# Performance work log

Measured on AMD Instinct MI355X. Metric: run time of the kernel, lower is better.

## Reference

```python
import jax, jax.numpy as jnp
import numpy as np

DIM = 512
HEADS = 8
DIM_HEAD = 64
INNER = HEADS * DIM_HEAD
SCALE = DIM_HEAD ** -0.5


def setup_inputs() -> dict:
    key = jax.random.key(0)
    ks = jax.random.split(key, 7)
    B, N = 8, 1024
    x = jax.random.normal(ks[0], (B, N, DIM), dtype=jnp.float32)
    rel_pos_bias = jax.random.normal(ks[1], (HEADS, N, N), dtype=jnp.float32) * 0.02
    w_qkv = jax.random.normal(ks[2], (DIM, 3 * INNER), dtype=jnp.float32) * (DIM ** -0.5)
    w_out = jax.random.normal(ks[3], (INNER, DIM), dtype=jnp.float32) * (INNER ** -0.5)
    b_out = jnp.zeros((DIM,), dtype=jnp.float32)
    ln_gamma = jnp.ones((DIM,), dtype=jnp.float32)
    ln_beta = jnp.zeros((DIM,), dtype=jnp.float32)
    return {"x": x, "rel_pos_bias": rel_pos_bias, "w_qkv": w_qkv,
            "w_out": w_out, "b_out": b_out, "ln_gamma": ln_gamma, "ln_beta": ln_beta}


def _layernorm(x, gamma, beta, eps=1e-5):
    mu = jnp.mean(x, axis=-1, keepdims=True)
    var = jnp.var(x, axis=-1, keepdims=True)
    return (x - mu) * jax.lax.rsqrt(var + eps) * gamma + beta


def reference(x, rel_pos_bias, w_qkv, w_out, b_out, ln_gamma, ln_beta):
    B, N, _ = x.shape
    xn = _layernorm(x, ln_gamma, ln_beta)
    qkv = xn @ w_qkv  # [B,N,3*INNER]
    q, k, v = jnp.split(qkv, 3, axis=-1)
    # b n (h d) -> b h n d
    reshape = lambda t: t.reshape(B, N, HEADS, DIM_HEAD).transpose(0, 2, 1, 3)
    q, k, v = reshape(q) * SCALE, reshape(k), reshape(v)
    sim = jnp.einsum('bhid,bhjd->bhij', q, k)
    sim = sim + rel_pos_bias  # broadcast [h,N,N] over batch
    attn = jax.nn.softmax(sim, axis=-1)
    out = jnp.einsum('bhij,bhjd->bhid', attn, v)
    out = out.transpose(0, 2, 1, 3).reshape(B, N, INNER)
    return out @ w_out + b_out
```

## Files before the change

### kernel.cpp

```cpp
#include <hip/hip_runtime.h>
#include <hip/hip_bf16.h>

#define DIM 512
#define HEADS 8
#define DHEAD 64
#define INNER 512
#define NSEQ 1024
#define BATCH 8
#define MROWS (BATCH*NSEQ)
#define QK_SCALE 0.125f

typedef __attribute__((ext_vector_type(4))) float f32x4;
typedef __attribute__((ext_vector_type(8))) short short8;
typedef unsigned short ushort_t;

__device__ inline ushort_t f2bf(float f) {
    __hip_bfloat16 h = __float2bfloat16(f);
    return *reinterpret_cast<ushort_t*>(&h);
}

__global__ __launch_bounds__(256) void ln_kernel(const float* __restrict__ x,
        const float* __restrict__ gamma, const float* __restrict__ beta,
        ushort_t* __restrict__ xn) {
    int row = blockIdx.x * 4 + (threadIdx.x >> 6);
    int lane = threadIdx.x & 63;
    const float4* xr = (const float4*)(x + (size_t)row * DIM);
    float4 a0 = xr[lane];
    float4 a1 = xr[lane + 64];
    float s  = a0.x + a0.y + a0.z + a0.w + a1.x + a1.y + a1.z + a1.w;
    float ss = a0.x*a0.x + a0.y*a0.y + a0.z*a0.z + a0.w*a0.w
             + a1.x*a1.x + a1.y*a1.y + a1.z*a1.z + a1.w*a1.w;
    for (int off = 1; off < 64; off <<= 1) {
        s  += __shfl_xor(s, off);
        ss += __shfl_xor(ss, off);
    }
    float mean = s * (1.0f / DIM);
    float var  = ss * (1.0f / DIM) - mean * mean;
    float inv  = rsqrtf(var + 1e-5f);
    const float4* g4 = (const float4*)gamma;
    const float4* b4 = (const float4*)beta;
    float4 g0 = g4[lane], g1 = g4[lane + 64];
    float4 be0 = b4[lane], be1 = b4[lane + 64];
    ushort4 o0, o1;
    o0.x = f2bf((a0.x - mean) * inv * g0.x + be0.x);
    o0.y = f2bf((a0.y - mean) * inv * g0.y + be0.y);
    o0.z = f2bf((a0.z - mean) * inv * g0.z + be0.z);
    o0.w = f2bf((a0.w - mean) * inv * g0.w + be0.w);
    o1.x = f2bf((a1.x - mean) * inv * g1.x + be1.x);
    o1.y = f2bf((a1.y - mean) * inv * g1.y + be1.y);
    o1.z = f2bf((a1.z - mean) * inv * g1.z + be1.z);
    o1.w = f2bf((a1.w - mean) * inv * g1.w + be1.w);
    ushort4* outr = (ushort4*)(xn + (size_t)row * DIM);
    outr[lane] = o0;
    outr[lane + 64] = o1;
}

__global__ __launch_bounds__(256) void transpose_cast(const float* __restrict__ w,
        ushort_t* __restrict__ wt, int ncols) {
    int idx = blockIdx.x * 256 + threadIdx.x;
    int n = idx >> 9, k = idx & 511;
    wt[idx] = f2bf(w[(size_t)k * ncols + n]);
}

template<int EPI>
__global__ __launch_bounds__(256) void gemm_kernel(
        const ushort_t* __restrict__ A, const ushort_t* __restrict__ Bt,
        ushort_t* __restrict__ qb, ushort_t* __restrict__ kb, ushort_t* __restrict__ vb,
        float* __restrict__ outp, const float* __restrict__ bvec) {
    __shared__ ushort_t Als[128][40];
    __shared__ ushort_t Bls[128][40];
    int t = threadIdx.x;
    int bm = blockIdx.y, bn = blockIdx.x;
    int lane = t & 63, w = t >> 6, wm = w >> 1, wn = w & 1;
    int l15 = lane & 15, l4 = lane >> 4;
    f32x4 acc[4][4] = {};

    for (int kt = 0; kt < DIM / 32; ++kt) {
        __syncthreads();
        {
            int row = t >> 2, c8 = (t & 3) * 8;
            uint4 va0 = *(const uint4*)(A  + (size_t)(bm*128 + row)      * DIM + kt*32 + c8);
            uint4 va1 = *(const uint4*)(A  + (size_t)(bm*128 + row + 64) * DIM + kt*32 + c8);
            uint4 vb0 = *(const uint4*)(Bt + (size_t)(bn*128 + row)      * DIM + kt*32 + c8);
            uint4 vb1 = *(const uint4*)(Bt + (size_t)(bn*128 + row + 64) * DIM + kt*32 + c8);
            *(uint4*)&Als[row][c8]      = va0;
            *(uint4*)&Als[row + 64][c8] = va1;
            *(uint4*)&Bls[row][c8]      = vb0;
            *(uint4*)&Bls[row + 64][c8] = vb1;
        }
        __syncthreads();
        short8 af[4], bfr[4];
        for (int mi = 0; mi < 4; mi++) af[mi]  = *(const short8*)&Als[wm*64 + mi*16 + l15][l4*8];
        for (int ni = 0; ni < 4; ni++) bfr[ni] = *(const short8*)&Bls[wn*64 + ni*16 + l15][l4*8];
        for (int mi = 0; mi < 4; mi++)
            for (int ni = 0; ni < 4; ni++)
                acc[mi][ni] = __builtin_amdgcn_mfma_f32_16x16x32_bf16(af[mi], bfr[ni], acc[mi][ni], 0, 0, 0);
    }

    int rbase = bm*128 + wm*64 + l4*4;
    int cbase = bn*128 + wn*64 + l15;
    for (int mi = 0; mi < 4; mi++)
        for (int ni = 0; ni < 4; ni++) {
            int c = cbase + ni*16;
            for (int j = 0; j < 4; j++) {
                int r = rbase + mi*16 + j;
                float val = acc[mi][ni][j];
                if (EPI == 0) {
                    int part = c >> 9, cw = c & 511;
                    int h = cw >> 6, d = cw & 63;
                    int b = r >> 10, i = r & 1023;
                    size_t off = (((size_t)(b*HEADS + h)) * NSEQ + i) * DHEAD + d;
                    if (part == 0)      qb[off] = f2bf(val * QK_SCALE);
                    else if (part == 1) kb[off] = f2bf(val);
                    else                vb[off] = f2bf(val);
                } else {
                    outp[(size_t)r * DIM + c] = val + bvec[c];
                }
            }
        }
}

__global__ __launch_bounds__(256) void attn_kernel(
        const ushort_t* __restrict__ q, const ushort_t* __restrict__ k,
        const ushort_t* __restrict__ v, const float* __restrict__ bias,
        ushort_t* __restrict__ attno) {
    __shared__ ushort_t Kls[64][72];
    __shared__ ushort_t Vtls[64][72];
    __shared__ ushort_t Pls[4][16][72];
    int t = threadIdx.x, lane = t & 63, w = t >> 6;
    int l15 = lane & 15, l4 = lane >> 4;
    int b = blockIdx.z, h = blockIdx.y, q0 = blockIdx.x * 64;
    const ushort_t* qp = q + (((size_t)(b*HEADS + h)) * NSEQ + q0 + w*16) * DHEAD;
    const ushort_t* kp = k + ((size_t)(b*HEADS + h)) * NSEQ * DHEAD;
    const ushort_t* vp = v + ((size_t)(b*HEADS + h)) * NSEQ * DHEAD;
    const float* bp = bias + (size_t)h * NSEQ * NSEQ;

    short8 aq[2];
    aq[0] = *(const short8*)(qp + l15*DHEAD + l4*8);
    aq[1] = *(const short8*)(qp + l15*DHEAD + l4*8 + 32);

    f32x4 o[4] = {};
    float mrun[4], lrun[4];
    for (int j = 0; j < 4; j++) { mrun[j] = -INFINITY; lrun[j] = 0.f; }
    int rbase = q0 + w*16 + l4*4;

    for (int kt = 0; kt < NSEQ / 64; ++kt) {
        __syncthreads();
        {
            int row = t >> 3, c8 = (t & 7) * 8;
            for (int r2 = 0; r2 < 2; ++r2) {
                int rr = row + r2*32;
                uint4 kv4 = *(const uint4*)(kp + (size_t)(kt*64 + rr) * DHEAD + c8);
                *(uint4*)&Kls[rr][c8] = kv4;
                uint4 vv4 = *(const uint4*)(vp + (size_t)(kt*64 + rr) * DHEAD + c8);
                ushort_t* vs = (ushort_t*)&vv4;
                for (int jj = 0; jj < 8; jj++) Vtls[c8 + jj][rr] = vs[jj];
            }
        }
        __syncthreads();

        f32x4 s[4] = {};
        for (int ni = 0; ni < 4; ni++)
            for (int ks = 0; ks < 2; ks++) {
                short8 bk = *(const short8*)&Kls[ni*16 + l15][l4*8 + 32*ks];
                s[ni] = __builtin_amdgcn_mfma_f32_16x16x32_bf16(aq[ks], bk, s[ni], 0, 0, 0);
            }

        float pv[4][4];
        const float* bpp = bp + (size_t)rbase * NSEQ + kt*64 + l15;
        for (int j = 0; j < 4; j++) {
            float mj = -INFINITY;
            for (int ni = 0; ni < 4; ni++) {
                float val = s[ni][j] + bpp[(size_t)j * NSEQ + ni*16];
                pv[ni][j] = val;
                mj = fmaxf(mj, val);
            }
            for (int off = 1; off < 16; off <<= 1) mj = fmaxf(mj, __shfl_xor(mj, off));
            float mnew = fmaxf(mrun[j], mj);
            float scl = __expf(mrun[j] - mnew);
            float rs = 0.f;
            for (int ni = 0; ni < 4; ni++) {
                float p = __expf(pv[ni][j] - mnew);
                pv[ni][j] = p;
                rs += p;
            }
            for (int off = 1; off < 16; off <<= 1) rs += __shfl_xor(rs, off);
            lrun[j] = lrun[j] * scl + rs;
            mrun[j] = mnew;
            for (int di = 0; di < 4; di++) o[di][j] *= scl;
        }

        for (int ni = 0; ni < 4; ni++)
            for (int j = 0; j < 4; j++)
                Pls[w][l4*4 + j][ni*16 + l15] = f2bf(pv[ni][j]);

        for (int ks = 0; ks < 2; ks++) {
            short8 pa = *(const short8*)&Pls[w][l15][l4*8 + 32*ks];
            for (int di = 0; di < 4; di++) {
                short8 bv = *(const short8*)&Vtls[di*16 + l15][l4*8 + 32*ks];
                o[di] = __builtin_amdgcn_mfma_f32_16x16x32_bf16(pa, bv, o[di], 0, 0, 0);
            }
        }
    }

    for (int di = 0; di < 4; di++)
        for (int j = 0; j < 4; j++) {
            int row = rbase + j;
            float val = o[di][j] / lrun[j];
            attno[((size_t)(b*NSEQ + row)) * INNER + h*DHEAD + di*16 + l15] = f2bf(val);
        }
}

extern "C" void kernel_launch(void* const* d_in, const int* in_sizes, int n_in,
                              void* d_out, int out_size, void* d_ws, size_t ws_size,
                              hipStream_t stream) {
    (void)in_sizes; (void)n_in; (void)out_size; (void)ws_size;
    const float* x      = (const float*)d_in[0];
    const float* bias   = (const float*)d_in[1];
    const float* w_qkv  = (const float*)d_in[2];
    const float* w_out  = (const float*)d_in[3];
    const float* b_out  = (const float*)d_in[4];
    const float* gamma  = (const float*)d_in[5];
    const float* beta   = (const float*)d_in[6];
    float* out = (float*)d_out;

    ushort_t* xn    = (ushort_t*)d_ws;
    ushort_t* wqkvT = xn + (size_t)MROWS * DIM;
    ushort_t* woutT = wqkvT + (size_t)1536 * 512;
    ushort_t* qb    = woutT + (size_t)512 * 512;
    ushort_t* kb    = qb + (size_t)MROWS * INNER;
    ushort_t* vb    = kb + (size_t)MROWS * INNER;
    ushort_t* attn  = vb + (size_t)MROWS * INNER;

    hipLaunchKernelGGL(ln_kernel, dim3(MROWS / 4), dim3(256), 0, stream, x, gamma, beta, xn);
    hipLaunchKernelGGL(transpose_cast, dim3(1536 * 512 / 256), dim3(256), 0, stream, w_qkv, wqkvT, 3 * INNER);
    hipLaunchKernelGGL(transpose_cast, dim3(512 * 512 / 256), dim3(256), 0, stream, w_out, woutT, DIM);
    hipLaunchKernelGGL((gemm_kernel<0>), dim3(1536 / 128, MROWS / 128), dim3(256), 0, stream,
                       xn, wqkvT, qb, kb, vb, nullptr, nullptr);
    hipLaunchKernelGGL(attn_kernel, dim3(NSEQ / 64, HEADS, BATCH), dim3(256), 0, stream,
                       qb, kb, vb, bias, attn);
    hipLaunchKernelGGL((gemm_kernel<1>), dim3(DIM / 128, MROWS / 128), dim3(256), 0, stream,
                       attn, woutT, nullptr, nullptr, nullptr, out, b_out);
}
```

Baseline: 225.2 us.

## Transpose attention MFMAs, pre-transpose V, and pre-convert bias to bf16

Swaps the MFMA operand roles in the attention kernel so each lane owns a whole query row. Row max and sum then need only two cross-lane shuffles, and bias loads become vectorized ushort4 reads along the key dimension. A separate kernel pre-transposes V into [bh, d, seq] layout, which replaces the scalar LDS transpose scatter with vector copies. Another kernel converts the rel_pos_bias to bf16 once per call, halving bias read traffic in attention. The cost is two extra launches and a full fp32 pass over the bias, plus bf16 rounding of the bias.

```diff
diff --git a/kernel.cpp b/kernel.cpp
--- a/kernel.cpp
+++ b/kernel.cpp
@@ -17,6 +17,9 @@
 __device__ inline ushort_t f2bf(float f) {
     __hip_bfloat16 h = __float2bfloat16(f);
     return *reinterpret_cast<ushort_t*>(&h);
+}
+__device__ inline float bf2f(ushort_t u) {
+    union { unsigned int i; float f; } c; c.i = ((unsigned int)u) << 16; return c.f;
 }
 
 __global__ __launch_bounds__(256) void ln_kernel(const float* __restrict__ x,
@@ -62,6 +65,34 @@
     wt[idx] = f2bf(w[(size_t)k * ncols + n]);
 }
 
+__global__ __launch_bounds__(256) void bias_cvt(const float* __restrict__ in,
+        ushort_t* __restrict__ out) {
+    int i = blockIdx.x * 256 + threadIdx.x;
+    float4 v = ((const float4*)in)[i];
+    ushort4 o;
+    o.x = f2bf(v.x); o.y = f2bf(v.y); o.z = f2bf(v.z); o.w = f2bf(v.w);
+    ((ushort4*)out)[i] = o;
+}
+
+__global__ __launch_bounds__(256) void v_transpose(const ushort_t* __restrict__ vb,
+        ushort_t* __restrict__ vt) {
+    __shared__ ushort_t T[64][72];
+    int bh = blockIdx.y;
+    int s0 = blockIdx.x * 64;
+    int t = threadIdx.x;
+    int row = t >> 2, c = (t & 3) * 16;
+    const ushort_t* src = vb + ((size_t)bh * NSEQ + s0 + row) * DHEAD + c;
+    *(uint4*)&T[row][c]     = *(const uint4*)(src);
+    *(uint4*)&T[row][c + 8] = *(const uint4*)(src + 8);
+    __syncthreads();
+    int d = t >> 2;
+    int sq = (t & 3) * 16;
+    ushort_t tmp[16];
+    for (int j = 0; j < 16; j++) tmp[j] = T[sq + j][d];
+    *(uint4*)(vt + ((size_t)bh * DHEAD + d) * NSEQ + s0 + sq)     = *(uint4*)&tmp[0];
+    *(uint4*)(vt + ((size_t)bh * DHEAD + d) * NSEQ + s0 + sq + 8) = *(uint4*)&tmp[8];
+}
+
 template<int EPI>
 __global__ __launch_bounds__(256) void gemm_kernel(
         const ushort_t* __restrict__ A, const ushort_t* __restrict__ Bt,
@@ -122,7 +153,7 @@
 
 __global__ __launch_bounds__(256) void attn_kernel(
         const ushort_t* __restrict__ q, const ushort_t* __restrict__ k,
-        const ushort_t* __restrict__ v, const float* __restrict__ bias,
+        const ushort_t* __restrict__ vt, const ushort_t* __restrict__ biasb,
         ushort_t* __restrict__ attno) {
     __shared__ ushort_t Kls[64][72];
     __shared__ ushort_t Vtls[64][72];
@@ -130,85 +161,95 @@
     int t = threadIdx.x, lane = t & 63, w = t >> 6;
     int l15 = lane & 15, l4 = lane >> 4;
     int b = blockIdx.z, h = blockIdx.y, q0 = blockIdx.x * 64;
-    const ushort_t* qp = q + (((size_t)(b*HEADS + h)) * NSEQ + q0 + w*16) * DHEAD;
-    const ushort_t* kp = k + ((size_t)(b*HEADS + h)) * NSEQ * DHEAD;
-    const ushort_t* vp = v + ((size_t)(b*HEADS + h)) * NSEQ * DHEAD;
-    const float* bp = bias + (size_t)h * NSEQ * NSEQ;
-
-    short8 aq[2];
-    aq[0] = *(const short8*)(qp + l15*DHEAD + l4*8);
-    aq[1] = *(const short8*)(qp + l15*DHEAD + l4*8 + 32);
+    size_t bh = (size_t)(b * HEADS + h);
+    const ushort_t* qp = q  + (bh * NSEQ + q0 + w*16) * DHEAD;
+    const ushort_t* kp = k  + bh * NSEQ * DHEAD;
+    const ushort_t* vp = vt + bh * DHEAD * NSEQ;
+    int qrow = q0 + w*16 + l15;
+    const ushort_t* bp = biasb + ((size_t)h * NSEQ + qrow) * NSEQ;
+
+    short8 bq[2];
+    bq[0] = *(const short8*)(qp + l15*DHEAD + l4*8);
+    bq[1] = *(const short8*)(qp + l15*DHEAD + l4*8 + 32);
 
     f32x4 o[4] = {};
-    float mrun[4], lrun[4];
-    for (int j = 0; j < 4; j++) { mrun[j] = -INFINITY; lrun[j] = 0.f; }
-    int rbase = q0 + w*16 + l4*4;
+    float mrun = -INFINITY, lrun = 0.f;
+
+    int srow = t >> 2, sc = (t & 3) * 16;
 
     for (int kt = 0; kt < NSEQ / 64; ++kt) {
         __syncthreads();
         {
-            int row = t >> 3, c8 = (t & 7) * 8;
-            for (int r2 = 0; r2 < 2; ++r2) {
-                int rr = row + r2*32;
-                uint4 kv4 = *(const uint4*)(kp + (size_t)(kt*64 + rr) * DHEAD + c8);
-                *(uint4*)&Kls[rr][c8] = kv4;
-                uint4 vv4 = *(const uint4*)(vp + (size_t)(kt*64 + rr) * DHEAD + c8);
-                ushort_t* vs = (ushort_t*)&vv4;
-                for (int jj = 0; jj < 8; jj++) Vtls[c8 + jj][rr] = vs[jj];
+            const ushort_t* ks = kp + (size_t)(kt*64 + srow) * DHEAD + sc;
+            const ushort_t* vs = vp + (size_t)srow * NSEQ + kt*64 + sc;
+            *(uint4*)&Kls[srow][sc]      = *(const uint4*)(ks);
+            *(uint4*)&Kls[srow][sc + 8]  = *(const uint4*)(ks + 8);
+            *(uint4*)&Vtls[srow][sc]     = *(const uint4*)(vs);
+            *(uint4*)&Vtls[srow][sc + 8] = *(const uint4*)(vs + 8);
+        }
+        __syncthreads();
+
+        f32x4 s[4];
+        for (int ni = 0; ni < 4; ni++) {
+            f32x4 z = {};
+            short8 ak0 = *(const short8*)&Kls[ni*16 + l15][l4*8];
+            short8 ak1 = *(const short8*)&Kls[ni*16 + l15][l4*8 + 32];
+            z = __builtin_amdgcn_mfma_f32_16x16x32_bf16(ak0, bq[0], z, 0, 0, 0);
+            z = __builtin_amdgcn_mfma_f32_16x16x32_bf16(ak1, bq[1], z, 0, 0, 0);
+            s[ni] = z;
+        }
+
+        float p[16];
+        float mj = -INFINITY;
+        for (int ni = 0; ni < 4; ni++) {
+            ushort4 b4 = *(const ushort4*)(bp + kt*64 + ni*16 + l4*4);
+            float v0 = s[ni][0] + bf2f(b4.x);
+            float v1 = s[ni][1] + bf2f(b4.y);
+            float v2 = s[ni][2] + bf2f(b4.z);
+            float v3 = s[ni][3] + bf2f(b4.w);
+            p[ni*4+0] = v0; p[ni*4+1] = v1; p[ni*4+2] = v2; p[ni*4+3] = v3;
+            mj = fmaxf(mj, fmaxf(fmaxf(v0, v1), fmaxf(v2, v3)));
+        }
+        mj = fmaxf(mj, __shfl_xor(mj, 16));
+        mj = fmaxf(mj, __shfl_xor(mj, 32));
+        float mnew = fmaxf(mrun, mj);
+        float scl = __expf(mrun - mnew);
+        float rs = 0.f;
+        for (int i = 0; i < 16; i++) {
+            p[i] = __expf(p[i] - mnew);
+            rs += p[i];
+        }
+        rs += __shfl_xor(rs, 16);
+        rs += __shfl_xor(rs, 32);
+        lrun = lrun * scl + rs;
+        mrun = mnew;
+        for (int di = 0; di < 4; di++) o[di] *= scl;
+
+        for (int ni = 0; ni < 4; ni++) {
+            ushort4 pk;
+            pk.x = f2bf(p[ni*4+0]); pk.y = f2bf(p[ni*4+1]);
+            pk.z = f2bf(p[ni*4+2]); pk.w = f2bf(p[ni*4+3]);
+            *(ushort4*)&Pls[w][l15][ni*16 + l4*4] = pk;
+        }
+
+        for (int ks2 = 0; ks2 < 2; ks2++) {
+            short8 pb = *(const short8*)&Pls[w][l15][ks2*32 + l4*8];
+            for (int di = 0; di < 4; di++) {
+                short8 av = *(const short8*)&Vtls[di*16 + l15][ks2*32 + l4*8];
+                o[di] = __builtin_amdgcn_mfma_f32_16x16x32_bf16(av, pb, o[di], 0, 0, 0);
             }
         }
-        __syncthreads();
-
-        f32x4 s[4] = {};
-        for (int ni = 0; ni < 4; ni++)
-            for (int ks = 0; ks < 2; ks++) {
-                short8 bk = *(const short8*)&Kls[ni*16 + l15][l4*8 + 32*ks];
-                s[ni] = __builtin_amdgcn_mfma_f32_16x16x32_bf16(aq[ks], bk, s[ni], 0, 0, 0);
-            }
-
-        float pv[4][4];
-        const float* bpp = bp + (size_t)rbase * NSEQ + kt*64 + l15;
-        for (int j = 0; j < 4; j++) {
-            float mj = -INFINITY;
-            for (int ni = 0; ni < 4; ni++) {
-                float val = s[ni][j] + bpp[(size_t)j * NSEQ + ni*16];
-                pv[ni][j] = val;
-                mj = fmaxf(mj, val);
-            }
-            for (int off = 1; off < 16; off <<= 1) mj = fmaxf(mj, __shfl_xor(mj, off));
-            float mnew = fmaxf(mrun[j], mj);
-            float scl = __expf(mrun[j] - mnew);
-            float rs = 0.f;
-            for (int ni = 0; ni < 4; ni++) {
-                float p = __expf(pv[ni][j] - mnew);
-                pv[ni][j] = p;
-                rs += p;
-            }
-            for (int off = 1; off < 16; off <<= 1) rs += __shfl_xor(rs, off);
-            lrun[j] = lrun[j] * scl + rs;
-            mrun[j] = mnew;
-            for (int di = 0; di < 4; di++) o[di][j] *= scl;
-        }
-
-        for (int ni = 0; ni < 4; ni++)
-            for (int j = 0; j < 4; j++)
-                Pls[w][l4*4 + j][ni*16 + l15] = f2bf(pv[ni][j]);
-
-        for (int ks = 0; ks < 2; ks++) {
-            short8 pa = *(const short8*)&Pls[w][l15][l4*8 + 32*ks];
-            for (int di = 0; di < 4; di++) {
-                short8 bv = *(const short8*)&Vtls[di*16 + l15][l4*8 + 32*ks];
-                o[di] = __builtin_amdgcn_mfma_f32_16x16x32_bf16(pa, bv, o[di], 0, 0, 0);
-            }
-        }
-    }
-
-    for (int di = 0; di < 4; di++)
-        for (int j = 0; j < 4; j++) {
-            int row = rbase + j;
-            float val = o[di][j] / lrun[j];
-            attno[((size_t)(b*NSEQ + row)) * INNER + h*DHEAD + di*16 + l15] = f2bf(val);
-        }
+    }
+
+    float inv = 1.0f / lrun;
+    for (int di = 0; di < 4; di++) {
+        ushort4 ov;
+        ov.x = f2bf(o[di][0] * inv);
+        ov.y = f2bf(o[di][1] * inv);
+        ov.z = f2bf(o[di][2] * inv);
+        ov.w = f2bf(o[di][3] * inv);
+        *(ushort4*)(attno + ((size_t)(b*NSEQ + qrow)) * INNER + h*DHEAD + di*16 + l4*4) = ov;
+    }
 }
 
 extern "C" void kernel_launch(void* const* d_in, const int* in_sizes, int n_in,
@@ -230,15 +271,19 @@
     ushort_t* qb    = woutT + (size_t)512 * 512;
     ushort_t* kb    = qb + (size_t)MROWS * INNER;
     ushort_t* vb    = kb + (size_t)MROWS * INNER;
-    ushort_t* attn  = vb + (size_t)MROWS * INNER;
+    ushort_t* vt    = vb + (size_t)MROWS * INNER;
+    ushort_t* attn  = vt + (size_t)MROWS * INNER;
+    ushort_t* biasb = attn + (size_t)MROWS * INNER;
 
     hipLaunchKernelGGL(ln_kernel, dim3(MROWS / 4), dim3(256), 0, stream, x, gamma, beta, xn);
     hipLaunchKernelGGL(transpose_cast, dim3(1536 * 512 / 256), dim3(256), 0, stream, w_qkv, wqkvT, 3 * INNER);
     hipLaunchKernelGGL(transpose_cast, dim3(512 * 512 / 256), dim3(256), 0, stream, w_out, woutT, DIM);
+    hipLaunchKernelGGL(bias_cvt, dim3(HEADS * NSEQ * NSEQ / 4 / 256), dim3(256), 0, stream, bias, biasb);
     hipLaunchKernelGGL((gemm_kernel<0>), dim3(1536 / 128, MROWS / 128), dim3(256), 0, stream,
                        xn, wqkvT, qb, kb, vb, nullptr, nullptr);
+    hipLaunchKernelGGL(v_transpose, dim3(NSEQ / 64, BATCH * HEADS), dim3(256), 0, stream, vb, vt);
     hipLaunchKernelGGL(attn_kernel, dim3(NSEQ / 64, HEADS, BATCH), dim3(256), 0, stream,
-                       qb, kb, vb, bias, attn);
+                       qb, kb, vt, biasb, attn);
     hipLaunchKernelGGL((gemm_kernel<1>), dim3(DIM / 128, MROWS / 128), dim3(256), 0, stream,
                        attn, woutT, nullptr, nullptr, nullptr, out, b_out);
 }
```

After: 211.3 us. 1.07x faster.
